# Kernel optimization log

Hardware: AMD Instinct MI355X
Metric: run time of the kernel (lower is better)

## Reference

```python
import jax, jax.numpy as jnp
import numpy as np

LN_EPS = 1e-5   # nn.LayerNorm default eps
EPS = 1e-3      # norm epsilon in module

B, R, S, C, CO, OUT = 1, 256, 128, 256, 32, 128  # res, seq, c_m, outer_channel, output_channel


def setup_inputs() -> dict:
    key = jax.random.key(0)
    ks = jax.random.split(key, 6)
    act = jax.random.normal(ks[0], (B, R, S, C), jnp.float32)
    mask = jnp.ones((B, S, R), jnp.float32)
    ln_gamma = jnp.ones((C,), jnp.float32)
    ln_beta = jnp.zeros((C,), jnp.float32)
    w_left = jax.random.normal(ks[1], (CO, C), jnp.float32) * (1.0 / np.sqrt(C))
    b_left = jnp.zeros((CO,), jnp.float32)
    w_right = jax.random.normal(ks[2], (CO, C), jnp.float32) * (1.0 / np.sqrt(C))
    b_right = jnp.zeros((CO,), jnp.float32)
    w_o = jax.random.normal(ks[3], (OUT, CO * CO), jnp.float32) * (1.0 / np.sqrt(CO * CO))
    b_o = jnp.zeros((OUT,), jnp.float32)
    return {"act": act, "mask": mask, "ln_gamma": ln_gamma, "ln_beta": ln_beta,
            "w_left": w_left, "b_left": b_left, "w_right": w_right, "b_right": b_right,
            "w_o": w_o, "b_o": b_o}


def reference(act, mask, ln_gamma, ln_beta, w_left, b_left, w_right, b_right, w_o, b_o):
    # act: [B, R(res), S(seq), C]; mask: [B, S, R]
    x = jnp.swapaxes(act, -3, -2)                     # permute_final_dims (1,0,2) -> [B, S, R, C]
    mu = x.mean(-1, keepdims=True)
    var = x.var(-1, keepdims=True)
    xn = (x - mu) * jax.lax.rsqrt(var + LN_EPS) * ln_gamma + ln_beta
    m = mask[..., None]                               # [B, S, R, 1]
    left = m * (xn @ w_left.T + b_left)               # [B, S, R, CO]
    right = m * (xn @ w_right.T + b_right)            # [B, S, R, CO]
    # outer product mean over seq dim: out[b,i,j,c,d] = sum_s left[b,s,i,c] * right[b,s,j,d]
    op = jnp.einsum('bsic,bsjd->bijcd', left, right)  # [B, R, R, CO, CO]
    op = op.reshape(op.shape[:3] + (CO * CO,))        # flatten_final_dims(.., 2)
    out = op @ w_o.T + b_o                            # [B, R, R, OUT]
    norm = jnp.einsum('bsi,bsj->bij', mask, mask)[..., None]  # [B, R, R, 1]
    return out / (EPS + norm)
```

## Files before the change

### kernel.cpp

```cpp
#include <hip/hip_runtime.h>
#include <hip/hip_bf16.h>
#include <stdint.h>

#define R_ 256
#define S_ 128
#define C_ 256
#define CO_ 32
#define OUT_ 128
#define LN_EPS 1e-5f
#define EPS_ 1e-3f

typedef __attribute__((ext_vector_type(8))) short bf16x8;
typedef __attribute__((ext_vector_type(4))) float f32x4;
typedef __attribute__((address_space(1))) const unsigned int GAS;
typedef __attribute__((address_space(3))) unsigned int LAS;

static __device__ __forceinline__ unsigned short f2bf(float f) {
  union { float f; uint32_t u; } cv; cv.f = f;
  uint32_t u = cv.u;
  uint32_t r = (u + 0x7FFFu + ((u >> 16) & 1u)) >> 16;
  return (unsigned short)r;
}

__global__ __launch_bounds__(256) void k_prep(
    const float* wl, const float* wr, const float* gamma, const float* beta,
    const float* bl, const float* br, const float* wo, const float* mask,
    unsigned short* wcat, float* g1, float* g0, float* bcat,
    unsigned short* wob2, float* invn) {
  int bid = blockIdx.x, tid = threadIdx.x;
  if (bid < 64) {
    int co = bid, c = tid;
    const float* src = (co < 32) ? (wl + co * C_) : (wr + (co - 32) * C_);
    float w = src[c], g = gamma[c], bt = beta[c];
    float wg = w * g;
    wcat[co * C_ + c] = f2bf(wg);
    __shared__ float red1[256], red0[256];
    red1[c] = wg; red0[c] = w * bt;
    __syncthreads();
    for (int off = 128; off > 0; off >>= 1) {
      if (c < off) { red1[c] += red1[c + off]; red0[c] += red0[c + off]; }
      __syncthreads();
    }
    if (c == 0) {
      g1[co] = red1[0]; g0[co] = red0[0];
      bcat[co] = (co < 32) ? bl[co] : br[co - 32];
    }
  } else if (bid < 192) {
    int o = bid - 64;
    float4 v = ((const float4*)wo)[o * 256 + tid];
    float vv[4] = {v.x, v.y, v.z, v.w};
#pragma unroll
    for (int e = 0; e < 4; ++e) {
      int kk = tid * 4 + e;
      int kk2 = (kk & 31) * 32 + (kk >> 5);
      wob2[(kk2 >> 3) * 1024 + o * 8 + (kk2 & 7)] = f2bf(vv[e]);
    }
  } else {
    int i = bid - 192, j = tid;
    float a = 0.f;
    for (int s = 0; s < S_; ++s) a += mask[s * R_ + i] * mask[s * R_ + j];
    invn[i * R_ + j] = 1.0f / (EPS_ + a);
  }
}

#define AP2 264
__global__ __launch_bounds__(256, 2) void k_proj(
    const float* __restrict__ act, const float* __restrict__ mask,
    const unsigned short* __restrict__ wcat,
    const float* __restrict__ g1v, const float* __restrict__ g0v,
    const float* __restrict__ bcv,
    unsigned short* __restrict__ leftg, unsigned short* __restrict__ rightg) {
  __shared__ __align__(16) unsigned short a_bf[64 * AP2];
  __shared__ __align__(16) unsigned short w_l[64 * AP2];
  __shared__ __align__(16) unsigned short trans[64 * 72];
  __shared__ float mu_s[64], rs_s[64], mk_s[64];
  __shared__ float g1s[64], g0s[64], bcs[64];
  int tid = threadIdx.x;
  int lane = tid & 63, w = tid >> 6;
  int r = blockIdx.x >> 1;
  int sh = (blockIdx.x & 1) * 64;

  const float4* actv = (const float4*)act;
  for (int it = 0; it < 16; ++it) {
    int s = w + it * 4;
    float4 v = actv[(size_t)r * 8192 + (size_t)(sh + s) * 64 + lane];
    float ls = v.x + v.y + v.z + v.w;
    float lq = v.x * v.x + v.y * v.y + v.z * v.z + v.w * v.w;
#pragma unroll
    for (int off = 32; off > 0; off >>= 1) {
      ls += __shfl_xor(ls, off);
      lq += __shfl_xor(lq, off);
    }
    if (lane == 0) {
      float mu = ls * (1.0f / 256.0f);
      float var = lq * (1.0f / 256.0f) - mu * mu;
      mu_s[s] = mu;
      rs_s[s] = rsqrtf(var + LN_EPS);
    }
    ushort4 o;
    o.x = f2bf(v.x); o.y = f2bf(v.y); o.z = f2bf(v.z); o.w = f2bf(v.w);
    *(ushort4*)&a_bf[s * AP2 + lane * 4] = o;
  }
  const uint4* wsrc = (const uint4*)wcat;
  for (int it = 0; it < 8; ++it) {
    int f = tid + it * 256;
    int co = f >> 5, ch = f & 31;
    *(uint4*)&w_l[co * AP2 + ch * 8] = wsrc[f];
  }
  if (tid < 64) {
    mk_s[tid] = mask[(size_t)(sh + tid) * R_ + r];
    g1s[tid] = g1v[tid]; g0s[tid] = g0v[tid]; bcs[tid] = bcv[tid];
  }
  __syncthreads();

  int l15 = lane & 15, l4 = lane >> 4;
  f32x4 acc[4];
#pragma unroll
  for (int b = 0; b < 4; ++b) acc[b] = (f32x4){0.f, 0.f, 0.f, 0.f};
  for (int ks = 0; ks < 8; ++ks) {
    bf16x8 af = *(const bf16x8*)&a_bf[(w * 16 + l15) * AP2 + ks * 32 + l4 * 8];
#pragma unroll
    for (int nf = 0; nf < 4; ++nf) {
      bf16x8 bfr = *(const bf16x8*)&w_l[(nf * 16 + l15) * AP2 + ks * 32 + l4 * 8];
      acc[nf] = __builtin_amdgcn_mfma_f32_16x16x32_bf16(af, bfr, acc[nf], 0, 0, 0);
    }
  }
#pragma unroll
  for (int nf = 0; nf < 4; ++nf) {
    int co = nf * 16 + l15;
    float G1 = g1s[co], G0 = g0s[co], BC = bcs[co];
#pragma unroll
    for (int reg = 0; reg < 4; ++reg) {
      int s = w * 16 + l4 * 4 + reg;
      float v = rs_s[s] * acc[nf][reg] - mu_s[s] * rs_s[s] * G1 + G0 + BC;
      v *= mk_s[s];
      trans[co * 72 + s] = f2bf(v);
    }
  }
  __syncthreads();

  for (int it2 = 0; it2 < 2; ++it2) {
    int idx = tid + it2 * 256;
    int row = idx >> 3, ch = idx & 7;
    uint4 val = *(const uint4*)&trans[row * 72 + ch * 8];
    if (row < 32)
      ((uint4*)leftg)[((size_t)(r * 32 + row)) * 16 + (sh >> 3) + ch] = val;
    else
      ((uint4*)rightg)[((size_t)(r * 32 + row - 32)) * 16 + (sh >> 3) + ch] = val;
  }
}

__global__ __launch_bounds__(512, 2) void k_main(
    const unsigned short* __restrict__ leftg, const unsigned short* __restrict__ rightg,
    const unsigned short* __restrict__ wob2, const float* __restrict__ bo,
    const float* __restrict__ invn, float* __restrict__ out) {
  __shared__ __align__(16) unsigned char smem[131072];
  unsigned char* opbytes = smem;
  unsigned short* opu16 = (unsigned short*)smem;
  float* redf = (float*)smem;
  int tid = threadIdx.x;
  int lane = tid & 63, w = tid >> 6;
  int l15 = lane & 15, l4 = lane >> 4;
  int bi = blockIdx.x >> 5, bj = blockIdx.x & 31;

  {
    const unsigned char* gA = (const unsigned char*)leftg + (size_t)bi * 65536;
    const unsigned char* gB = (const unsigned char*)rightg + (size_t)bj * 65536;
#pragma unroll
    for (int k = 0; k < 8; ++k) {
      int rowbase = w * 32 + k * 4;
      int row = rowbase + (lane >> 4);
      int ch = (lane & 15) ^ (row & 7);
      __builtin_amdgcn_global_load_lds((GAS*)(gA + row * 256 + ch * 16),
                                       (LAS*)&smem[rowbase * 256], 16, 0, 0);
      __builtin_amdgcn_global_load_lds((GAS*)(gB + row * 256 + ch * 16),
                                       (LAS*)&smem[65536 + rowbase * 256], 16, 0, 0);
    }
  }
  __syncthreads();

  int wm = w >> 2, wn = w & 3;
  f32x4 acc[8][4];
#pragma unroll
  for (int a = 0; a < 8; ++a)
#pragma unroll
    for (int b = 0; b < 4; ++b) acc[a][b] = (f32x4){0.f, 0.f, 0.f, 0.f};
  for (int ks = 0; ks < 4; ++ks) {
    bf16x8 af[8], bfr[4];
#pragma unroll
    for (int mf = 0; mf < 8; ++mf) {
      int row = wm * 128 + mf * 16 + l15;
      int ch = (ks * 4 + l4) ^ (row & 7);
      af[mf] = *(const bf16x8*)&smem[row * 256 + ch * 16];
    }
#pragma unroll
    for (int nf = 0; nf < 4; ++nf) {
      int row = wn * 64 + nf * 16 + l15;
      int ch = (ks * 4 + l4) ^ (row & 7);
      bfr[nf] = *(const bf16x8*)&smem[65536 + row * 256 + ch * 16];
    }
#pragma unroll
    for (int mf = 0; mf < 8; ++mf)
#pragma unroll
      for (int nf = 0; nf < 4; ++nf)
        acc[mf][nf] = __builtin_amdgcn_mfma_f32_16x16x32_bf16(af[mf], bfr[nf], acc[mf][nf], 0, 0, 0);
  }
  __syncthreads();

#pragma unroll
  for (int mf = 0; mf < 8; ++mf) {
#pragma unroll
    for (int nf = 0; nf < 4; ++nf) {
      int p = (wm * 4 + (mf >> 1)) * 8 + wn * 2 + (nf >> 1);
      int d = ((nf & 1) << 4) + l15;
      int c0 = ((mf & 1) << 4) + l4 * 4;
      int baddr = p * 2048 + ((d * 64 + c0 * 2) ^ ((p & 7) << 4));
      uint32_t h0 = f2bf(acc[mf][nf][0]), h1 = f2bf(acc[mf][nf][1]);
      uint32_t h2 = f2bf(acc[mf][nf][2]), h3 = f2bf(acc[mf][nf][3]);
      uint2 pk; pk.x = h0 | (h1 << 16); pk.y = h2 | (h3 << 16);
      *(uint2*)&opbytes[baddr] = pk;
    }
  }
  __syncthreads();

  int kh = w >> 2, wn2 = w & 3;
  f32x4 acc2[4][2];
#pragma unroll
  for (int a = 0; a < 4; ++a) { acc2[a][0] = (f32x4){0,0,0,0}; acc2[a][1] = (f32x4){0,0,0,0}; }
  {
    const uint4* wv = (const uint4*)wob2;
    int ks0 = kh * 16;
#pragma unroll 2
    for (int ks2 = ks0; ks2 < ks0 + 16; ++ks2) {
      uint4 b0r = wv[(ks2 * 4 + l4) * 128 + wn2 * 32 + l15];
      uint4 b1r = wv[(ks2 * 4 + l4) * 128 + wn2 * 32 + 16 + l15];
      bf16x8 b0 = *(const bf16x8*)&b0r;
      bf16x8 b1 = *(const bf16x8*)&b1r;
      bf16x8 a2[4];
#pragma unroll
      for (int mf = 0; mf < 4; ++mf) {
        int p = mf * 16 + l15;
        int ch = (ks2 * 4 + l4) ^ (p & 7);
        a2[mf] = *(const bf16x8*)&opu16[p * 1024 + ch * 8];
      }
#pragma unroll
      for (int mf = 0; mf < 4; ++mf) {
        acc2[mf][0] = __builtin_amdgcn_mfma_f32_16x16x32_bf16(a2[mf], b0, acc2[mf][0], 0, 0, 0);
        acc2[mf][1] = __builtin_amdgcn_mfma_f32_16x16x32_bf16(a2[mf], b1, acc2[mf][1], 0, 0, 0);
      }
    }
  }
  __syncthreads();

  if (kh == 1) {
#pragma unroll
    for (int mf = 0; mf < 4; ++mf)
#pragma unroll
      for (int n2 = 0; n2 < 2; ++n2)
        *(f32x4*)&redf[((w - 4) * 64 + lane) * 36 + (mf * 2 + n2) * 4] = acc2[mf][n2];
  }
  __syncthreads();
  if (kh == 0) {
#pragma unroll
    for (int mf = 0; mf < 4; ++mf)
#pragma unroll
      for (int n2 = 0; n2 < 2; ++n2) {
        f32x4 pv = *(const f32x4*)&redf[(w * 64 + lane) * 36 + (mf * 2 + n2) * 4];
        acc2[mf][n2] += pv;
      }
#pragma unroll
    for (int n2 = 0; n2 < 2; ++n2) {
      int o = wn2 * 32 + n2 * 16 + l15;
      float bov = bo[o];
#pragma unroll
      for (int mf = 0; mf < 4; ++mf) {
#pragma unroll
        for (int reg = 0; reg < 4; ++reg) {
          int p = mf * 16 + l4 * 4 + reg;
          int gi = bi * 8 + (p >> 3), gj = bj * 8 + (p & 7);
          float v = (acc2[mf][n2][reg] + bov) * invn[gi * R_ + gj];
          out[((size_t)(gi * R_ + gj)) * OUT_ + o] = v;
        }
      }
    }
  }
}

extern "C" void kernel_launch(void* const* d_in, const int* in_sizes, int n_in,
                              void* d_out, int out_size, void* d_ws, size_t ws_size,
                              hipStream_t stream) {
  (void)in_sizes; (void)n_in; (void)out_size; (void)ws_size;
  const float* act   = (const float*)d_in[0];
  const float* mask  = (const float*)d_in[1];
  const float* gamma = (const float*)d_in[2];
  const float* beta  = (const float*)d_in[3];
  const float* wl    = (const float*)d_in[4];
  const float* bl    = (const float*)d_in[5];
  const float* wr    = (const float*)d_in[6];
  const float* br    = (const float*)d_in[7];
  const float* wo    = (const float*)d_in[8];
  const float* bo    = (const float*)d_in[9];
  float* out = (float*)d_out;
  unsigned char* ws = (unsigned char*)d_ws;
  unsigned short* leftg  = (unsigned short*)(ws + 0);
  unsigned short* rightg = (unsigned short*)(ws + 2097152);
  unsigned short* wob2   = (unsigned short*)(ws + 4194304);
  float* invn            = (float*)(ws + 4456448);
  unsigned short* wcat   = (unsigned short*)(ws + 4718592);
  float* g1              = (float*)(ws + 4751360);
  float* g0              = (float*)(ws + 4751616);
  float* bcat            = (float*)(ws + 4751872);

  hipLaunchKernelGGL(k_prep, dim3(448), dim3(256), 0, stream,
                     wl, wr, gamma, beta, bl, br, wo, mask,
                     wcat, g1, g0, bcat, wob2, invn);
  hipLaunchKernelGGL(k_proj, dim3(512), dim3(256), 0, stream,
                     act, mask, wcat, g1, g0, bcat, leftg, rightg);
  hipLaunchKernelGGL(k_main, dim3(1024), dim3(512), 0, stream,
                     leftg, rightg, wob2, bo, invn, out);
}
```

Baseline: 160.1 us.

## Rework LDS swizzle, prefetch W_o, move LN stats to LDS pass, stage invn/bias

Several changes land at once. The outer-product LDS tile gets a new XOR swizzle that also mixes in d and ks, to reduce bank conflicts on the bf16 writes and reads. The W_o fragment loads in the second GEMM are now software-prefetched one step ahead, and that loop is unrolled 4 instead of 2. The LayerNorm mean and variance move out of the per-row shuffle reduction into a separate pass over the bf16 tile in LDS, which means the statistics are now computed from rounded values. invn and b_o are staged in shared memory, the W_o prep uses vector stores, and the launch_bounds occupancy hint for k_main drops from 2 to 1, which may change register allocation.

```diff
diff --git a/kernel.cpp b/kernel.cpp
--- a/kernel.cpp
+++ b/kernel.cpp
@@ -47,17 +47,22 @@
     }
   } else if (bid < 192) {
     int o = bid - 64;
-    float4 v = ((const float4*)wo)[o * 256 + tid];
-    float vv[4] = {v.x, v.y, v.z, v.w};
-#pragma unroll
-    for (int e = 0; e < 4; ++e) {
-      int kk = tid * 4 + e;
-      int kk2 = (kk & 31) * 32 + (kk >> 5);
-      wob2[(kk2 >> 3) * 1024 + o * 8 + (kk2 & 7)] = f2bf(vv[e]);
+    if (tid < 128) {
+      int q = tid;
+      const float* row = wo + (size_t)o * 1024;
+      int dd = q >> 2, cb = (q & 3) * 8;
+      ushort4 lo, hi;
+      lo.x = f2bf(row[(cb + 0) * 32 + dd]); lo.y = f2bf(row[(cb + 1) * 32 + dd]);
+      lo.z = f2bf(row[(cb + 2) * 32 + dd]); lo.w = f2bf(row[(cb + 3) * 32 + dd]);
+      hi.x = f2bf(row[(cb + 4) * 32 + dd]); hi.y = f2bf(row[(cb + 5) * 32 + dd]);
+      hi.z = f2bf(row[(cb + 6) * 32 + dd]); hi.w = f2bf(row[(cb + 7) * 32 + dd]);
+      *(ushort4*)&wob2[q * 1024 + o * 8] = lo;
+      *(ushort4*)&wob2[q * 1024 + o * 8 + 4] = hi;
     }
   } else {
     int i = bid - 192, j = tid;
     float a = 0.f;
+#pragma unroll 8
     for (int s = 0; s < S_; ++s) a += mask[s * R_ + i] * mask[s * R_ + j];
     invn[i * R_ + j] = 1.0f / (EPS_ + a);
   }
@@ -73,6 +78,7 @@
   __shared__ __align__(16) unsigned short a_bf[64 * AP2];
   __shared__ __align__(16) unsigned short w_l[64 * AP2];
   __shared__ __align__(16) unsigned short trans[64 * 72];
+  __shared__ float psum[64][4], psq[64][4];
   __shared__ float mu_s[64], rs_s[64], mk_s[64];
   __shared__ float g1s[64], g0s[64], bcs[64];
   int tid = threadIdx.x;
@@ -84,19 +90,6 @@
   for (int it = 0; it < 16; ++it) {
     int s = w + it * 4;
     float4 v = actv[(size_t)r * 8192 + (size_t)(sh + s) * 64 + lane];
-    float ls = v.x + v.y + v.z + v.w;
-    float lq = v.x * v.x + v.y * v.y + v.z * v.z + v.w * v.w;
-#pragma unroll
-    for (int off = 32; off > 0; off >>= 1) {
-      ls += __shfl_xor(ls, off);
-      lq += __shfl_xor(lq, off);
-    }
-    if (lane == 0) {
-      float mu = ls * (1.0f / 256.0f);
-      float var = lq * (1.0f / 256.0f) - mu * mu;
-      mu_s[s] = mu;
-      rs_s[s] = rsqrtf(var + LN_EPS);
-    }
     ushort4 o;
     o.x = f2bf(v.x); o.y = f2bf(v.y); o.z = f2bf(v.z); o.w = f2bf(v.w);
     *(ushort4*)&a_bf[s * AP2 + lane * 4] = o;
@@ -110,6 +103,35 @@
   if (tid < 64) {
     mk_s[tid] = mask[(size_t)(sh + tid) * R_ + r];
     g1s[tid] = g1v[tid]; g0s[tid] = g0v[tid]; bcs[tid] = bcv[tid];
+  }
+  __syncthreads();
+
+  {
+    int row = tid >> 2, cc = tid & 3;
+    float sum = 0.f, sq = 0.f;
+#pragma unroll
+    for (int k = 0; k < 8; ++k) {
+      uint4 v = *(const uint4*)&a_bf[row * AP2 + cc * 8 + k * 32];
+      uint32_t ws_[4] = {v.x, v.y, v.z, v.w};
+#pragma unroll
+      for (int qd = 0; qd < 4; ++qd) {
+        union { uint32_t u; float f; } lo, hi;
+        lo.u = ws_[qd] << 16;
+        hi.u = ws_[qd] & 0xFFFF0000u;
+        sum += lo.f + hi.f;
+        sq += lo.f * lo.f + hi.f * hi.f;
+      }
+    }
+    psum[row][cc] = sum; psq[row][cc] = sq;
+  }
+  __syncthreads();
+  if (tid < 64) {
+    float s4 = psum[tid][0] + psum[tid][1] + psum[tid][2] + psum[tid][3];
+    float q4 = psq[tid][0] + psq[tid][1] + psq[tid][2] + psq[tid][3];
+    float mu = s4 * (1.0f / 256.0f);
+    float var = q4 * (1.0f / 256.0f) - mu * mu;
+    mu_s[tid] = mu;
+    rs_s[tid] = rsqrtf(var + LN_EPS);
   }
   __syncthreads();
 
@@ -150,11 +172,13 @@
   }
 }
 
-__global__ __launch_bounds__(512, 2) void k_main(
+__global__ __launch_bounds__(512, 1) void k_main(
     const unsigned short* __restrict__ leftg, const unsigned short* __restrict__ rightg,
     const unsigned short* __restrict__ wob2, const float* __restrict__ bo,
     const float* __restrict__ invn, float* __restrict__ out) {
   __shared__ __align__(16) unsigned char smem[131072];
+  __shared__ float invt[64];
+  __shared__ float bos[128];
   unsigned char* opbytes = smem;
   unsigned short* opu16 = (unsigned short*)smem;
   float* redf = (float*)smem;
@@ -162,6 +186,11 @@
   int lane = tid & 63, w = tid >> 6;
   int l15 = lane & 15, l4 = lane >> 4;
   int bi = blockIdx.x >> 5, bj = blockIdx.x & 31;
+
+  if (tid < 64)
+    invt[tid] = invn[(size_t)(bi * 8 + (tid >> 3)) * R_ + bj * 8 + (tid & 7)];
+  else if (tid < 192)
+    bos[tid - 64] = bo[tid - 64];
 
   {
     const unsigned char* gA = (const unsigned char*)leftg + (size_t)bi * 65536;
@@ -213,8 +242,9 @@
     for (int nf = 0; nf < 4; ++nf) {
       int p = (wm * 4 + (mf >> 1)) * 8 + wn * 2 + (nf >> 1);
       int d = ((nf & 1) << 4) + l15;
-      int c0 = ((mf & 1) << 4) + l4 * 4;
-      int baddr = p * 2048 + ((d * 64 + c0 * 2) ^ ((p & 7) << 4));
+      int q = d * 4 + ((mf & 1) << 1) + (l4 >> 1);
+      int sc = q ^ (p & 7) ^ (d & 7);
+      int baddr = p * 2048 + sc * 16 + (l4 & 1) * 8;
       uint32_t h0 = f2bf(acc[mf][nf][0]), h1 = f2bf(acc[mf][nf][1]);
       uint32_t h2 = f2bf(acc[mf][nf][2]), h3 = f2bf(acc[mf][nf][3]);
       uint2 pk; pk.x = h0 | (h1 << 16); pk.y = h2 | (h3 << 16);
@@ -230,18 +260,24 @@
   {
     const uint4* wv = (const uint4*)wob2;
     int ks0 = kh * 16;
-#pragma unroll 2
+    uint4 b0n = wv[(ks0 * 4 + l4) * 128 + wn2 * 32 + l15];
+    uint4 b1n = wv[(ks0 * 4 + l4) * 128 + wn2 * 32 + 16 + l15];
+#pragma unroll 4
     for (int ks2 = ks0; ks2 < ks0 + 16; ++ks2) {
-      uint4 b0r = wv[(ks2 * 4 + l4) * 128 + wn2 * 32 + l15];
-      uint4 b1r = wv[(ks2 * 4 + l4) * 128 + wn2 * 32 + 16 + l15];
+      uint4 b0r = b0n, b1r = b1n;
+      if (ks2 + 1 < ks0 + 16) {
+        b0n = wv[((ks2 + 1) * 4 + l4) * 128 + wn2 * 32 + l15];
+        b1n = wv[((ks2 + 1) * 4 + l4) * 128 + wn2 * 32 + 16 + l15];
+      }
       bf16x8 b0 = *(const bf16x8*)&b0r;
       bf16x8 b1 = *(const bf16x8*)&b1r;
       bf16x8 a2[4];
 #pragma unroll
       for (int mf = 0; mf < 4; ++mf) {
         int p = mf * 16 + l15;
-        int ch = (ks2 * 4 + l4) ^ (p & 7);
-        a2[mf] = *(const bf16x8*)&opu16[p * 1024 + ch * 8];
+        int q = ks2 * 4 + l4;
+        int sc = q ^ (p & 7) ^ (ks2 & 7);
+        a2[mf] = *(const bf16x8*)&opu16[p * 1024 + sc * 8];
       }
 #pragma unroll
       for (int mf = 0; mf < 4; ++mf) {
@@ -271,14 +307,14 @@
 #pragma unroll
     for (int n2 = 0; n2 < 2; ++n2) {
       int o = wn2 * 32 + n2 * 16 + l15;
-      float bov = bo[o];
+      float bov = bos[o];
 #pragma unroll
       for (int mf = 0; mf < 4; ++mf) {
 #pragma unroll
         for (int reg = 0; reg < 4; ++reg) {
           int p = mf * 16 + l4 * 4 + reg;
           int gi = bi * 8 + (p >> 3), gj = bj * 8 + (p & 7);
-          float v = (acc2[mf][n2][reg] + bov) * invn[gi * R_ + gj];
+          float v = (acc2[mf][n2][reg] + bov) * invt[p];
           out[((size_t)(gi * R_ + gj)) * OUT_ + o] = v;
         }
       }
```

Result: faster. 150.0 us (-6.3%).
